# Optimization experiments

Hardware: AMD Instinct MI355X
Metric: run time of the kernel (lower is better)

## Reference

```python
import jax, jax.numpy as jnp
import numpy as np

# torch semantics: m = x > 0; y = x[m]  (flattened stream compaction);
# unsqueeze(0) then squeeze([0]) is an identity.
# JAX/jit cannot return data-dependent shapes, so we return the compacted
# values moved to the front of a fixed-size buffer (padded with 0) plus the
# valid count. y_padded[:count] == torch's y.

def reference(x):
    xf = x.reshape(-1)                      # [N]
    mask = xf > 0.0                         # [N] bool
    count = jnp.sum(mask)                   # scalar int: number of valid elems
    # stable argsort on ~mask moves True-mask positions to the front,
    # preserving original order (matches masked_select ordering)
    order = jnp.argsort(jnp.logical_not(mask), stable=True)  # [N]
    n = xf.shape[0]
    y_padded = jnp.where(jnp.arange(n) < count, xf[order], 0.0)  # [N]
    return y_padded, count


def setup_inputs() -> dict:
    key = jax.random.key(0)
    x = jax.random.normal(key, (64, 1024, 1024), dtype=jnp.float32)
    return {"x": x}
```

## Files before the change

### kernel.cpp

```cpp
#include <hip/hip_runtime.h>


#define BLOCK 256
#define VPT 16
#define CHUNK (BLOCK * VPT)
#define SCAN_THREADS 1024
#define SCAN_VPT 16

typedef float floatx4 __attribute__((ext_vector_type(4)));

__global__ void __launch_bounds__(BLOCK)
k_count(const float* __restrict__ x, int n, int* __restrict__ blockSums) {
    const int tid = threadIdx.x;
    const long long chunkBase = (long long)blockIdx.x * CHUNK;
    int cnt = 0;
    if (chunkBase + CHUNK <= n) {
        const float* p = x + chunkBase + tid * 4;
#pragma unroll
        for (int it = 0; it < 4; ++it) {
            const float4 v = *reinterpret_cast<const float4*>(p + it * (BLOCK * 4));
            cnt += (v.x > 0.f) + (v.y > 0.f) + (v.z > 0.f) + (v.w > 0.f);
        }
    } else {
        const long long lim = (chunkBase + CHUNK < n) ? chunkBase + CHUNK : n;
        for (long long j = chunkBase + tid; j < lim; j += BLOCK) cnt += (x[j] > 0.f);
    }
#pragma unroll
    for (int off = 32; off > 0; off >>= 1) cnt += __shfl_down(cnt, off, 64);
    __shared__ int lds[4];
    if ((tid & 63) == 0) lds[tid >> 6] = cnt;
    __syncthreads();
    if (tid == 0) blockSums[blockIdx.x] = lds[0] + lds[1] + lds[2] + lds[3];
}

__global__ void k_scan(int* __restrict__ sums, int numBlocks,
                       int* __restrict__ countOut, float* __restrict__ countOutF) {
    __shared__ int lds[32];
    const int tid  = threadIdx.x;
    const int lane = tid & 63;
    const int wave = tid >> 6;

    int vals[SCAN_VPT];
    const int base = tid * SCAN_VPT;
    int local = 0;
#pragma unroll
    for (int j = 0; j < SCAN_VPT; ++j) {
        const int i = base + j;
        const int v = (i < numBlocks) ? sums[i] : 0;
        vals[j] = local;
        local += v;
    }
    int incl = local;
#pragma unroll
    for (int off = 1; off < 64; off <<= 1) {
        const int y = __shfl_up(incl, off, 64);
        if (lane >= off) incl += y;
    }
    if (lane == 63) lds[wave] = incl;
    __syncthreads();
    if (wave == 0 && lane < 16) {
        int w = lds[lane];
#pragma unroll
        for (int off = 1; off < 16; off <<= 1) {
            const int y = __shfl_up(w, off, 16);
            if ((lane & 15) >= off) w += y;
        }
        lds[16 + lane] = w;
    }
    __syncthreads();
    const int waveEx   = (wave == 0) ? 0 : lds[16 + wave - 1];
    const int threadEx = waveEx + incl - local;
#pragma unroll
    for (int j = 0; j < SCAN_VPT; ++j) {
        const int i = base + j;
        if (i < numBlocks) sums[i] = threadEx + vals[j];
    }
    if (tid == SCAN_THREADS - 1) {
        const int total = waveEx + incl;
        *countOut  = total;
        *countOutF = (float)total;
    }
}

__device__ __forceinline__ int block_scan_excl_256(int val, int* lds, int* blockTotal) {
    const int tid  = threadIdx.x;
    const int lane = tid & 63;
    const int wave = tid >> 6;
    int incl = val;
#pragma unroll
    for (int off = 1; off < 64; off <<= 1) {
        const int y = __shfl_up(incl, off, 64);
        if (lane >= off) incl += y;
    }
    if (lane == 63) lds[wave] = incl;
    __syncthreads();
    if (tid == 0) {
        const int s0 = lds[0], s1 = lds[1], s2 = lds[2], s3 = lds[3];
        lds[4] = 0; lds[5] = s0; lds[6] = s0 + s1; lds[7] = s0 + s1 + s2;
        lds[8] = s0 + s1 + s2 + s3;
    }
    __syncthreads();
    const int ex = lds[4 + wave] + incl - val;
    *blockTotal = lds[8];
    return ex;
}

__global__ void __launch_bounds__(BLOCK)
k_scatter(const float* __restrict__ x, int n, int numBlocks,
          const int* __restrict__ blockOffsets, float* __restrict__ y) {
    __shared__ __align__(16) float vals[CHUNK + 4];
    __shared__ int scan_lds[9];
    const int tid = threadIdx.x;
    const int chunk = numBlocks - 1 - blockIdx.x;
    const int chunkBase = chunk * CHUNK;
    const long long tbase = (long long)chunkBase + tid * VPT;

    float v[VPT];
    if ((long long)chunkBase + CHUNK <= n) {
#pragma unroll
        for (int k = 0; k < 4; ++k) {
            const float4 f = *reinterpret_cast<const float4*>(x + tbase + 4 * k);
            v[4 * k + 0] = f.x; v[4 * k + 1] = f.y; v[4 * k + 2] = f.z; v[4 * k + 3] = f.w;
        }
    } else {
#pragma unroll
        for (int j = 0; j < VPT; ++j)
            v[j] = (tbase + j < n) ? x[tbase + j] : 0.f;
    }

    int c = 0;
#pragma unroll
    for (int j = 0; j < VPT; ++j) c += (v[j] > 0.f);

    int total;
    int r = block_scan_excl_256(c, scan_lds, &total);

    const int excl = blockOffsets[chunk];
    const int pad  = excl & 3;

    r += pad;
#pragma unroll
    for (int j = 0; j < VPT; ++j) {
        if (v[j] > 0.f) vals[r++] = v[j];
    }
    __syncthreads();

    const int m = pad + total;
    const long long yb = (long long)excl - pad;
    const int nq = (m + 3) >> 2;
    for (int t = tid; t < nq; t += BLOCK) {
        const int k0 = 4 * t;
        if (k0 >= pad && k0 + 4 <= m) {
            __builtin_nontemporal_store(
                *reinterpret_cast<const floatx4*>(&vals[k0]),
                reinterpret_cast<floatx4*>(y + yb + k0));
        } else {
            const int ks = (k0 < pad) ? pad : k0;
            const int ke = (k0 + 4 < m) ? k0 + 4 : m;
            for (int k = ks; k < ke; ++k)
                __builtin_nontemporal_store(vals[k], y + yb + k);
        }
    }

    const int rem   = n - chunkBase;
    const int elems = rem < CHUNK ? rem : CHUNK;
    const int z     = elems - total;
    const long long zhi = (long long)n - (chunkBase - excl);
    const long long zlo = zhi - z;
    const long long za  = (zlo + 3) & ~3LL;
    const long long zb  = zhi & ~3LL;
    if (za >= zb) {
        for (long long j = zlo + tid; j < zhi; j += BLOCK)
            __builtin_nontemporal_store(0.f, y + j);
    } else {
        if (tid < (int)(za - zlo))
            __builtin_nontemporal_store(0.f, y + zlo + tid);
        if (tid >= 4 && tid - 4 < (int)(zhi - zb))
            __builtin_nontemporal_store(0.f, y + zb + tid - 4);
        const int zq = (int)((zb - za) >> 2);
        const floatx4 zero = (floatx4)(0.f);
        for (int t = tid; t < zq; t += BLOCK) {
            __builtin_nontemporal_store(zero, reinterpret_cast<floatx4*>(y + za + 4 * t));
        }
    }
}

extern "C" void kernel_launch(void* const* d_in, const int* in_sizes, int n_in,
                              void* d_out, int out_size, void* d_ws, size_t ws_size,
                              hipStream_t stream) {
    const float* x = (const float*)d_in[0];
    float* y = (float*)d_out;
    const int n = in_sizes[0];

    int* blockSums = (int*)d_ws;
    const int numBlocks = (n + CHUNK - 1) / CHUNK;
    int* countPtr = blockSums + numBlocks;

    k_count<<<numBlocks, BLOCK, 0, stream>>>(x, n, blockSums);
    k_scan<<<1, SCAN_THREADS, 0, stream>>>(blockSums, numBlocks,
                                           countPtr, y + (out_size - 1));
    k_scatter<<<numBlocks, BLOCK, 0, stream>>>(x, n, numBlocks, blockSums, y);
}
```

Measured before the change: 480.4 us.

## Stage per-chunk compacted values in workspace instead of re-reading input for scatter

Replaces the count-only first pass with a staging kernel that compacts each chunk in LDS and writes the positive values to a per-chunk workspace slot, along with the block count. The emit kernel then reads only the compacted slot rather than re-reading and re-filtering the full input chunk. This cuts the second full read of the input, but adds a compacted-value write and read, so total traffic ends up roughly similar. It also needs a workspace as large as the input, which the workspace may not provide.

Result: slower. 516.4 us (+7.5%).

```diff
diff --git a/kernel.cpp b/kernel.cpp
--- a/kernel.cpp
+++ b/kernel.cpp
@@ -9,32 +9,76 @@
 
 typedef float floatx4 __attribute__((ext_vector_type(4)));
 
+__device__ __forceinline__ int block_scan_excl_256(int val, int* lds, int* blockTotal) {
+    const int tid  = threadIdx.x;
+    const int lane = tid & 63;
+    const int wave = tid >> 6;
+    int incl = val;
+#pragma unroll
+    for (int off = 1; off < 64; off <<= 1) {
+        const int y = __shfl_up(incl, off, 64);
+        if (lane >= off) incl += y;
+    }
+    if (lane == 63) lds[wave] = incl;
+    __syncthreads();
+    if (tid == 0) {
+        const int s0 = lds[0], s1 = lds[1], s2 = lds[2], s3 = lds[3];
+        lds[4] = 0; lds[5] = s0; lds[6] = s0 + s1; lds[7] = s0 + s1 + s2;
+        lds[8] = s0 + s1 + s2 + s3;
+    }
+    __syncthreads();
+    const int ex = lds[4 + wave] + incl - val;
+    *blockTotal = lds[8];
+    return ex;
+}
+
 __global__ void __launch_bounds__(BLOCK)
-k_count(const float* __restrict__ x, int n, int* __restrict__ blockSums) {
+k_stage(const float* __restrict__ x, int n, float* __restrict__ slots,
+        int* __restrict__ blockSums) {
+    __shared__ __align__(16) float vals[CHUNK];
+    __shared__ int scan_lds[9];
     const int tid = threadIdx.x;
     const long long chunkBase = (long long)blockIdx.x * CHUNK;
-    int cnt = 0;
+    const long long tbase = chunkBase + tid * VPT;
+
+    float v[VPT];
     if (chunkBase + CHUNK <= n) {
-        const float* p = x + chunkBase + tid * 4;
-#pragma unroll
-        for (int it = 0; it < 4; ++it) {
-            const float4 v = *reinterpret_cast<const float4*>(p + it * (BLOCK * 4));
-            cnt += (v.x > 0.f) + (v.y > 0.f) + (v.z > 0.f) + (v.w > 0.f);
+#pragma unroll
+        for (int k = 0; k < 4; ++k) {
+            const floatx4 f = __builtin_nontemporal_load(
+                reinterpret_cast<const floatx4*>(x + tbase + 4 * k));
+            v[4 * k + 0] = f.x; v[4 * k + 1] = f.y; v[4 * k + 2] = f.z; v[4 * k + 3] = f.w;
         }
     } else {
-        const long long lim = (chunkBase + CHUNK < n) ? chunkBase + CHUNK : n;
-        for (long long j = chunkBase + tid; j < lim; j += BLOCK) cnt += (x[j] > 0.f);
-    }
-#pragma unroll
-    for (int off = 32; off > 0; off >>= 1) cnt += __shfl_down(cnt, off, 64);
-    __shared__ int lds[4];
-    if ((tid & 63) == 0) lds[tid >> 6] = cnt;
-    __syncthreads();
-    if (tid == 0) blockSums[blockIdx.x] = lds[0] + lds[1] + lds[2] + lds[3];
+#pragma unroll
+        for (int j = 0; j < VPT; ++j)
+            v[j] = (tbase + j < n) ? x[tbase + j] : 0.f;
+    }
+
+    int c = 0;
+#pragma unroll
+    for (int j = 0; j < VPT; ++j) c += (v[j] > 0.f);
+
+    int total;
+    int r = block_scan_excl_256(c, scan_lds, &total);
+    if (tid == 0) blockSums[blockIdx.x] = total;
+
+#pragma unroll
+    for (int j = 0; j < VPT; ++j) {
+        if (v[j] > 0.f) vals[r++] = v[j];
+    }
+    __syncthreads();
+
+    float* slot = slots + chunkBase;
+    const int nq = (total + 3) >> 2;
+    for (int t = tid; t < nq; t += BLOCK) {
+        *reinterpret_cast<floatx4*>(slot + 4 * t) =
+            *reinterpret_cast<const floatx4*>(&vals[4 * t]);
+    }
 }
 
 __global__ void k_scan(int* __restrict__ sums, int numBlocks,
-                       int* __restrict__ countOut, float* __restrict__ countOutF) {
+                       float* __restrict__ countOutF) {
     __shared__ int lds[32];
     const int tid  = threadIdx.x;
     const int lane = tid & 63;
@@ -77,75 +121,34 @@
     }
     if (tid == SCAN_THREADS - 1) {
         const int total = waveEx + incl;
-        *countOut  = total;
+        sums[numBlocks] = total;
         *countOutF = (float)total;
     }
 }
 
-__device__ __forceinline__ int block_scan_excl_256(int val, int* lds, int* blockTotal) {
-    const int tid  = threadIdx.x;
-    const int lane = tid & 63;
-    const int wave = tid >> 6;
-    int incl = val;
-#pragma unroll
-    for (int off = 1; off < 64; off <<= 1) {
-        const int y = __shfl_up(incl, off, 64);
-        if (lane >= off) incl += y;
-    }
-    if (lane == 63) lds[wave] = incl;
-    __syncthreads();
-    if (tid == 0) {
-        const int s0 = lds[0], s1 = lds[1], s2 = lds[2], s3 = lds[3];
-        lds[4] = 0; lds[5] = s0; lds[6] = s0 + s1; lds[7] = s0 + s1 + s2;
-        lds[8] = s0 + s1 + s2 + s3;
-    }
-    __syncthreads();
-    const int ex = lds[4 + wave] + incl - val;
-    *blockTotal = lds[8];
-    return ex;
-}
-
 __global__ void __launch_bounds__(BLOCK)
-k_scatter(const float* __restrict__ x, int n, int numBlocks,
-          const int* __restrict__ blockOffsets, float* __restrict__ y) {
+k_emit(const float* __restrict__ slots, int n,
+       const int* __restrict__ offs, float* __restrict__ y) {
     __shared__ __align__(16) float vals[CHUNK + 4];
-    __shared__ int scan_lds[9];
     const int tid = threadIdx.x;
-    const int chunk = numBlocks - 1 - blockIdx.x;
-    const int chunkBase = chunk * CHUNK;
-    const long long tbase = (long long)chunkBase + tid * VPT;
-
-    float v[VPT];
-    if ((long long)chunkBase + CHUNK <= n) {
-#pragma unroll
-        for (int k = 0; k < 4; ++k) {
-            const float4 f = *reinterpret_cast<const float4*>(x + tbase + 4 * k);
-            v[4 * k + 0] = f.x; v[4 * k + 1] = f.y; v[4 * k + 2] = f.z; v[4 * k + 3] = f.w;
-        }
-    } else {
-#pragma unroll
-        for (int j = 0; j < VPT; ++j)
-            v[j] = (tbase + j < n) ? x[tbase + j] : 0.f;
-    }
-
-    int c = 0;
-#pragma unroll
-    for (int j = 0; j < VPT; ++j) c += (v[j] > 0.f);
-
-    int total;
-    int r = block_scan_excl_256(c, scan_lds, &total);
-
-    const int excl = blockOffsets[chunk];
+    const int b = blockIdx.x;
+    const long long chunkBase = (long long)b * CHUNK;
+
+    const int excl = offs[b];
+    const int cnt  = offs[b + 1] - excl;
     const int pad  = excl & 3;
 
-    r += pad;
-#pragma unroll
-    for (int j = 0; j < VPT; ++j) {
-        if (v[j] > 0.f) vals[r++] = v[j];
-    }
-    __syncthreads();
-
-    const int m = pad + total;
+    const float* slot = slots + chunkBase;
+    const int nqs = (cnt + 3) >> 2;
+    for (int t = tid; t < nqs; t += BLOCK) {
+        const floatx4 f = __builtin_nontemporal_load(
+            reinterpret_cast<const floatx4*>(slot + 4 * t));
+        const int k = pad + 4 * t;
+        vals[k] = f.x; vals[k + 1] = f.y; vals[k + 2] = f.z; vals[k + 3] = f.w;
+    }
+    __syncthreads();
+
+    const int m = pad + cnt;
     const long long yb = (long long)excl - pad;
     const int nq = (m + 3) >> 2;
     for (int t = tid; t < nq; t += BLOCK) {
@@ -162,9 +165,9 @@
         }
     }
 
-    const int rem   = n - chunkBase;
+    const int rem   = (int)(n - chunkBase);
     const int elems = rem < CHUNK ? rem : CHUNK;
-    const int z     = elems - total;
+    const int z     = elems - cnt;
     const long long zhi = (long long)n - (chunkBase - excl);
     const long long zlo = zhi - z;
     const long long za  = (zlo + 3) & ~3LL;
@@ -192,12 +195,11 @@
     float* y = (float*)d_out;
     const int n = in_sizes[0];
 
-    int* blockSums = (int*)d_ws;
     const int numBlocks = (n + CHUNK - 1) / CHUNK;
-    int* countPtr = blockSums + numBlocks;
-
-    k_count<<<numBlocks, BLOCK, 0, stream>>>(x, n, blockSums);
-    k_scan<<<1, SCAN_THREADS, 0, stream>>>(blockSums, numBlocks,
-                                           countPtr, y + (out_size - 1));
-    k_scatter<<<numBlocks, BLOCK, 0, stream>>>(x, n, numBlocks, blockSums, y);
-}
+    float* slots = (float*)d_ws;
+    int* blockSums = (int*)(slots + (long long)numBlocks * CHUNK);
+
+    k_stage<<<numBlocks, BLOCK, 0, stream>>>(x, n, slots, blockSums);
+    k_scan<<<1, SCAN_THREADS, 0, stream>>>(blockSums, numBlocks, y + (out_size - 1));
+    k_emit<<<numBlocks, BLOCK, 0, stream>>>(slots, n, blockSums, y);
+}
```

## Replace the separate scan kernel with per-block prefix reductions inside the scatter kernel

Applied to the files above, without the earlier changes.

Removes the single-block k_scan launch. Each scatter block now finds its output offset by summing the block counts of all earlier chunks, using a strided loop and a wave/LDS reduction. The last chunk writes the total count into the final output slot. This drops a serialized one-block kernel and a launch gap. In exchange, the block-count array is re-read roughly quadratically, up to ~16K ints per block across ~16K blocks, which adds substantial L2 traffic and per-block latency.

New measurement: 495.8 us. 1.03x slower.

```diff
diff --git a/kernel.cpp b/kernel.cpp
--- a/kernel.cpp
+++ b/kernel.cpp
@@ -4,8 +4,6 @@
 #define BLOCK 256
 #define VPT 16
 #define CHUNK (BLOCK * VPT)
-#define SCAN_THREADS 1024
-#define SCAN_VPT 16
 
 typedef float floatx4 __attribute__((ext_vector_type(4)));
 
@@ -33,55 +31,6 @@
     if (tid == 0) blockSums[blockIdx.x] = lds[0] + lds[1] + lds[2] + lds[3];
 }
 
-__global__ void k_scan(int* __restrict__ sums, int numBlocks,
-                       int* __restrict__ countOut, float* __restrict__ countOutF) {
-    __shared__ int lds[32];
-    const int tid  = threadIdx.x;
-    const int lane = tid & 63;
-    const int wave = tid >> 6;
-
-    int vals[SCAN_VPT];
-    const int base = tid * SCAN_VPT;
-    int local = 0;
-#pragma unroll
-    for (int j = 0; j < SCAN_VPT; ++j) {
-        const int i = base + j;
-        const int v = (i < numBlocks) ? sums[i] : 0;
-        vals[j] = local;
-        local += v;
-    }
-    int incl = local;
-#pragma unroll
-    for (int off = 1; off < 64; off <<= 1) {
-        const int y = __shfl_up(incl, off, 64);
-        if (lane >= off) incl += y;
-    }
-    if (lane == 63) lds[wave] = incl;
-    __syncthreads();
-    if (wave == 0 && lane < 16) {
-        int w = lds[lane];
-#pragma unroll
-        for (int off = 1; off < 16; off <<= 1) {
-            const int y = __shfl_up(w, off, 16);
-            if ((lane & 15) >= off) w += y;
-        }
-        lds[16 + lane] = w;
-    }
-    __syncthreads();
-    const int waveEx   = (wave == 0) ? 0 : lds[16 + wave - 1];
-    const int threadEx = waveEx + incl - local;
-#pragma unroll
-    for (int j = 0; j < SCAN_VPT; ++j) {
-        const int i = base + j;
-        if (i < numBlocks) sums[i] = threadEx + vals[j];
-    }
-    if (tid == SCAN_THREADS - 1) {
-        const int total = waveEx + incl;
-        *countOut  = total;
-        *countOutF = (float)total;
-    }
-}
-
 __device__ __forceinline__ int block_scan_excl_256(int val, int* lds, int* blockTotal) {
     const int tid  = threadIdx.x;
     const int lane = tid & 63;
@@ -106,11 +55,14 @@
 }
 
 __global__ void __launch_bounds__(BLOCK)
-k_scatter(const float* __restrict__ x, int n, int numBlocks,
-          const int* __restrict__ blockOffsets, float* __restrict__ y) {
+k_scatter(const float* __restrict__ x, int n, int numBlocks, int out_size,
+          const int* __restrict__ blockSums, float* __restrict__ y) {
     __shared__ __align__(16) float vals[CHUNK + 4];
     __shared__ int scan_lds[9];
-    const int tid = threadIdx.x;
+    __shared__ int red_lds[4];
+    const int tid  = threadIdx.x;
+    const int lane = tid & 63;
+    const int wave = tid >> 6;
     const int chunk = numBlocks - 1 - blockIdx.x;
     const int chunkBase = chunk * CHUNK;
     const long long tbase = (long long)chunkBase + tid * VPT;
@@ -128,16 +80,21 @@
             v[j] = (tbase + j < n) ? x[tbase + j] : 0.f;
     }
 
+    int psum = 0;
+    for (int i = tid; i < chunk; i += BLOCK) psum += blockSums[i];
+#pragma unroll
+    for (int off = 32; off > 0; off >>= 1) psum += __shfl_down(psum, off, 64);
+    if (lane == 0) red_lds[wave] = psum;
+
     int c = 0;
 #pragma unroll
     for (int j = 0; j < VPT; ++j) c += (v[j] > 0.f);
 
     int total;
     int r = block_scan_excl_256(c, scan_lds, &total);
+    const int excl = red_lds[0] + red_lds[1] + red_lds[2] + red_lds[3];
 
-    const int excl = blockOffsets[chunk];
-    const int pad  = excl & 3;
-
+    const int pad = excl & 3;
     r += pad;
 #pragma unroll
     for (int j = 0; j < VPT; ++j) {
@@ -183,6 +140,10 @@
             __builtin_nontemporal_store(zero, reinterpret_cast<floatx4*>(y + za + 4 * t));
         }
     }
+
+    if (chunk == numBlocks - 1 && tid == 0) {
+        y[out_size - 1] = (float)(excl + total);
+    }
 }
 
 extern "C" void kernel_launch(void* const* d_in, const int* in_sizes, int n_in,
@@ -194,10 +155,7 @@
 
     int* blockSums = (int*)d_ws;
     const int numBlocks = (n + CHUNK - 1) / CHUNK;
-    int* countPtr = blockSums + numBlocks;
 
     k_count<<<numBlocks, BLOCK, 0, stream>>>(x, n, blockSums);
-    k_scan<<<1, SCAN_THREADS, 0, stream>>>(blockSums, numBlocks,
-                                           countPtr, y + (out_size - 1));
-    k_scatter<<<numBlocks, BLOCK, 0, stream>>>(x, n, numBlocks, blockSums, y);
+    k_scatter<<<numBlocks, BLOCK, 0, stream>>>(x, n, numBlocks, out_size, blockSums, y);
 }
```
